# Optimization experiments

Hardware: AMD Instinct MI355X
Metric: run time of the kernel (lower is better)

The kernel has to match this reference:

```python
import jax, jax.numpy as jnp
import numpy as np

E, TOPK, D, F, FS = 16, 4, 2560, 1664, 3328
B, S = 1, 2048


def setup_inputs() -> dict:
    key = jax.random.key(0)
    ks = jax.random.split(key, 8)
    sc = lambda *sh: 1.0 / np.sqrt(sh[-2] if len(sh) > 1 else 1.0)
    return {
        "hidden_states": jax.random.normal(ks[0], (B, S, D), jnp.float32),
        "router_weight": jax.random.normal(ks[1], (E, D), jnp.float32) * (1.0 / np.sqrt(D)),
        "w_gate": jax.random.normal(ks[2], (E, D, F), jnp.float32) * (1.0 / np.sqrt(D)),
        "w_up": jax.random.normal(ks[3], (E, D, F), jnp.float32) * (1.0 / np.sqrt(D)),
        "w_down": jax.random.normal(ks[4], (E, F, D), jnp.float32) * (1.0 / np.sqrt(F)),
        "sw_gate": jax.random.normal(ks[5], (D, FS), jnp.float32) * (1.0 / np.sqrt(D)),
        "sw_up": jax.random.normal(ks[6], (D, FS), jnp.float32) * (1.0 / np.sqrt(D)),
        "sw_down": jax.random.normal(ks[7], (FS, D), jnp.float32) * (1.0 / np.sqrt(FS)),
    }


def reference(hidden_states, router_weight, w_gate, w_up, w_down, sw_gate, sw_up, sw_down):
    b, s, d = hidden_states.shape
    x = hidden_states.reshape(-1, d)  # [T, D]
    T = x.shape[0]

    # Router: linear -> softmax -> top-k -> renormalize (vLLM FusedMoE default)
    logits = x @ router_weight.T                      # [T, E]
    probs = jax.nn.softmax(logits, axis=-1)
    topk_w, topk_idx = jax.lax.top_k(probs, TOPK)     # [T, K]
    topk_w = topk_w / jnp.sum(topk_w, axis=-1, keepdims=True)
    combine = jnp.zeros((T, E), x.dtype).at[jnp.arange(T)[:, None], topk_idx].add(topk_w)  # [T, E]

    # Expert SiLU-gated MLPs (dense-dispatch reference for grouped GEMM)
    g = jnp.einsum('td,edf->tef', x, w_gate)          # [T, E, F]
    u = jnp.einsum('td,edf->tef', x, w_up)
    h = jax.nn.silu(g) * u
    y = jnp.einsum('tef,efd->ted', h, w_down)         # [T, E, D]
    sparse_out = jnp.einsum('ted,te->td', y, combine)

    # Shared expert: LlamaMLP with silu gate, no bias
    shared_out = (jax.nn.silu(x @ sw_gate) * (x @ sw_up)) @ sw_down

    return (sparse_out + shared_out).reshape(b, s, d)
```

## Files before the change

kernel.cpp:

```cpp
#include <hip/hip_runtime.h>
#include <hip/hip_bf16.h>
#include <stdint.h>

#define E_N 16
#define TOPK 4
#define DD 2560
#define FF 1664
#define FSS 3328
#define TT 2048

#define BM 128
#define BN 128
#define BK 32

typedef __attribute__((ext_vector_type(8))) __bf16 bf16x8;
typedef __attribute__((ext_vector_type(4))) float f32x4;

static_assert(DD % 64 == 0 && FF % 64 == 0 && FSS % 64 == 0, "64 divisibility");

__device__ __forceinline__ unsigned short f2bf(float f) {
  return __builtin_bit_cast(unsigned short, (__bf16)f);
}
__device__ __forceinline__ unsigned int pk2(float a, float b) {
  return (unsigned int)f2bf(a) | ((unsigned int)f2bf(b) << 16);
}

#define GLOAD16(g, l)                                                          \
  __builtin_amdgcn_global_load_lds(                                            \
      (const __attribute__((address_space(1))) void*)(g),                      \
      (__attribute__((address_space(3))) void*)(l), 16, 0, 0)

#define SBAR() __builtin_amdgcn_s_barrier()
#define SCHED0() __builtin_amdgcn_sched_barrier(0)
#define VMW(N) asm volatile("s_waitcnt vmcnt(" #N ")" ::: "memory")

__device__ __forceinline__ void swz_block(int& bm, int& bn, int& bz) {
  int gx = gridDim.x, gy = gridDim.y;
  int nwg = gx * gy * gridDim.z;
  int flat = blockIdx.x + gx * (blockIdx.y + gy * blockIdx.z);
  if ((nwg & 7) == 0) flat = (flat & 7) * (nwg >> 3) + (flat >> 3);
  bm = flat % gx;
  int rest = flat / gx;
  bn = rest % gy;
  bz = rest / gy;
}

__global__ __launch_bounds__(256) void cvt_bf16_kernel(const float* __restrict__ in,
                                                       unsigned short* __restrict__ out) {
  size_t i = ((size_t)blockIdx.x * 256 + threadIdx.x) * 4;
  float4 v = *reinterpret_cast<const float4*>(in + i);
  ushort4 o;
  o.x = f2bf(v.x); o.y = f2bf(v.y); o.z = f2bf(v.z); o.w = f2bf(v.w);
  *reinterpret_cast<ushort4*>(out + i) = o;
}

__global__ __launch_bounds__(256) void tcvt_kernel(const float* __restrict__ in,
                                                   unsigned short* __restrict__ out,
                                                   int K, int N) {
  __shared__ float lds[64 * 65];
  int z = blockIdx.z;
  in += (size_t)z * K * N;
  out += (size_t)z * K * N;
  int k0 = blockIdx.x * 64, n0 = blockIdx.y * 64;
  int t = threadIdx.x;
#pragma unroll
  for (int j = 0; j < 4; ++j) {
    int idx = j * 256 + t;
    int r = idx >> 4, c = (idx & 15) * 4;
    float4 v = *reinterpret_cast<const float4*>(in + (size_t)(k0 + r) * N + n0 + c);
    lds[r * 65 + c] = v.x;
    lds[r * 65 + c + 1] = v.y;
    lds[r * 65 + c + 2] = v.z;
    lds[r * 65 + c + 3] = v.w;
  }
  __syncthreads();
#pragma unroll
  for (int j = 0; j < 2; ++j) {
    int idx = j * 256 + t;
    int n = idx >> 3, kg = (idx & 7) * 8;
    float a0 = lds[(kg + 0) * 65 + n], a1 = lds[(kg + 1) * 65 + n];
    float a2 = lds[(kg + 2) * 65 + n], a3 = lds[(kg + 3) * 65 + n];
    float a4 = lds[(kg + 4) * 65 + n], a5 = lds[(kg + 5) * 65 + n];
    float a6 = lds[(kg + 6) * 65 + n], a7 = lds[(kg + 7) * 65 + n];
    uint4 o{pk2(a0, a1), pk2(a2, a3), pk2(a4, a5), pk2(a6, a7)};
    *reinterpret_cast<uint4*>(out + (size_t)(n0 + n) * K + k0 + kg) = o;
  }
}

__global__ __launch_bounds__(256) void router_kernel(const float* __restrict__ x,
                                                     const float* __restrict__ rw,
                                                     int* __restrict__ cnt,
                                                     int* __restrict__ list,
                                                     float* __restrict__ tw) {
  int t = blockIdx.x;
  const float* xr = x + (size_t)t * DD;
  __shared__ float logits[E_N];
  int lane = threadIdx.x & 63, wid = threadIdx.x >> 6;
  for (int ee = 0; ee < 4; ++ee) {
    int e = wid * 4 + ee;
    const float* wr = rw + (size_t)e * DD;
    float p = 0.f;
    for (int d = lane; d < DD; d += 64) p += xr[d] * wr[d];
#pragma unroll
    for (int off = 32; off > 0; off >>= 1) p += __shfl_down(p, off);
    if (lane == 0) logits[e] = p;
  }
  __syncthreads();
  if (threadIdx.x == 0) {
    float mx = -1e30f;
    for (int e = 0; e < E_N; ++e) mx = fmaxf(mx, logits[e]);
    float pe[E_N];
    for (int e = 0; e < E_N; ++e) pe[e] = __expf(logits[e] - mx);
    int idx[TOPK]; float val[TOPK]; float s4 = 0.f;
    unsigned used = 0;
    for (int k = 0; k < TOPK; ++k) {
      int bi = 0; float bv = -1.f;
      for (int e = 0; e < E_N; ++e)
        if (!((used >> e) & 1) && pe[e] > bv) { bv = pe[e]; bi = e; }
      used |= 1u << bi; idx[k] = bi; val[k] = bv; s4 += bv;
    }
    float inv = 1.f / s4;
    for (int k = 0; k < TOPK; ++k) {
      int e2 = idx[k];
      int pos = atomicAdd(&cnt[e2], 1);
      list[e2 * TT + pos] = t * 4 + k;
      tw[t * 4 + k] = val[k] * inv;
    }
  }
}

__global__ __launch_bounds__(256, 2) void gu_kernel(
    const unsigned short* __restrict__ Xb,
    const unsigned short* __restrict__ WgT,
    const unsigned short* __restrict__ WuT,
    unsigned short* __restrict__ H,
    const int* __restrict__ list, const int* __restrict__ cnt,
    int Ktot, int Ntot, int Mfixed) {
  int bm, bn, e;
  swz_block(bm, bn, e);
  int M = cnt ? cnt[e] : Mfixed;
  int m0 = bm * BM;
  if (m0 >= M) return;
  int n0 = bn * BN;
  const unsigned short* Bg0 = WgT + (size_t)e * Ktot * Ntot;
  const unsigned short* Bu0 = WuT + (size_t)e * Ktot * Ntot;
  const int* lst = list ? (list + e * TT) : nullptr;

  __shared__ __align__(16) unsigned short lds[3][12288];

  int tid = threadIdx.x, lane = tid & 63, w = tid >> 6;

  const unsigned short* pA[2];
#pragma unroll
  for (int q = 0; q < 2; ++q) {
    int J = w * 2 + q;
    int row = J * 16 + (lane >> 2);
    int c = lane & 3;
    int cs = c ^ (row & 3);
    int ar = min(m0 + row, M - 1);
    int tok = lst ? (lst[ar] >> 2) : ar;
    pA[q] = Xb + (size_t)tok * Ktot + cs * 8;
  }
  const unsigned short* pGU[4];
#pragma unroll
  for (int q = 0; q < 4; ++q) {
    int J = w * 4 + q;
    int row = J * 8 + (lane >> 3);
    int c = lane & 7;
    int sc = c ^ (row & 7);
    pGU[q] = (sc < 4) ? (Bg0 + (size_t)(n0 + row) * Ktot + sc * 8)
                      : (Bu0 + (size_t)(n0 + row) * Ktot + (sc - 4) * 8);
  }

  auto issue = [&](int kt, int buf) {
    int koff = kt * BK;
    unsigned short* dA = &lds[buf][0];
    unsigned short* dGU = &lds[buf][4096];
#pragma unroll
    for (int q = 0; q < 2; ++q)
      GLOAD16(pA[q] + koff, dA + (w * 2 + q) * 512);
#pragma unroll
    for (int q = 0; q < 4; ++q)
      GLOAD16(pGU[q] + koff, dGU + (w * 4 + q) * 512);
  };

  int wr = (w >> 1) * 64, wc = (w & 1) * 64;
  int cg = lane >> 4;
  int aoff[4], goff[4], uoff[4];
#pragma unroll
  for (int m = 0; m < 4; ++m) {
    int r = wr + m * 16 + (lane & 15);
    aoff[m] = r * 32 + ((cg ^ (r & 3)) * 8);
  }
#pragma unroll
  for (int n = 0; n < 4; ++n) {
    int r = wc + n * 16 + (lane & 15);
    goff[n] = r * 64 + ((cg ^ (r & 7)) * 8);
    uoff[n] = r * 64 + (((cg + 4) ^ (r & 7)) * 8);
  }

  f32x4 accG[4][4] = {};
  f32x4 accU[4][4] = {};

  auto compute = [&](int buf) {
    const unsigned short* A = &lds[buf][0];
    const unsigned short* GU = &lds[buf][4096];
    bf16x8 a[4], g[4], u[4];
#pragma unroll
    for (int m = 0; m < 4; ++m)
      a[m] = __builtin_bit_cast(bf16x8, *reinterpret_cast<const uint4*>(A + aoff[m]));
#pragma unroll
    for (int n = 0; n < 4; ++n) {
      g[n] = __builtin_bit_cast(bf16x8, *reinterpret_cast<const uint4*>(GU + goff[n]));
      u[n] = __builtin_bit_cast(bf16x8, *reinterpret_cast<const uint4*>(GU + uoff[n]));
    }
#pragma unroll
    for (int m = 0; m < 4; ++m)
#pragma unroll
      for (int n = 0; n < 4; ++n) {
        accG[m][n] = __builtin_amdgcn_mfma_f32_16x16x32_bf16(a[m], g[n], accG[m][n], 0, 0, 0);
        accU[m][n] = __builtin_amdgcn_mfma_f32_16x16x32_bf16(a[m], u[n], accU[m][n], 0, 0, 0);
      }
  };

  int nk = Ktot / BK;
  VMW(0); SCHED0();
  issue(0, 0);
  issue(1, 1);
  for (int kt = 0; kt < nk; ++kt) {
    if (kt + 2 < nk) { issue(kt + 2, (kt + 2) % 3); VMW(12); }
    else if (kt + 1 < nk) { VMW(6); }
    else { VMW(0); }
    SCHED0();
    SBAR(); SCHED0();
    compute(kt % 3);
    SCHED0();
    SBAR(); SCHED0();
  }

#pragma unroll
  for (int m = 0; m < 4; ++m) {
#pragma unroll
    for (int r = 0; r < 4; ++r) {
      int lr = wr + m * 16 + (lane >> 4) * 4 + r;
      int grow = m0 + lr;
      if (grow < M) {
        int code = lst ? lst[grow] : grow;
        unsigned short* Hp = H + (size_t)code * Ntot + n0 + wc + (lane & 15);
#pragma unroll
        for (int n = 0; n < 4; ++n) {
          float gg = accG[m][n][r], uu = accU[m][n][r];
          Hp[n * 16] = f2bf((gg / (1.f + __expf(-gg))) * uu);
        }
      }
    }
  }
}

__global__ __launch_bounds__(256, 3) void dn_kernel(
    const unsigned short* __restrict__ Hb,
    const unsigned short* __restrict__ WT,
    float* __restrict__ Y,
    const int* __restrict__ list, const int* __restrict__ cnt,
    const float* __restrict__ tw, int Ktot, int Ntot, int Mfixed) {
  int bm, bn, e;
  swz_block(bm, bn, e);
  int M = cnt ? cnt[e] : Mfixed;
  int m0 = bm * BM;
  if (m0 >= M) return;
  int n0 = bn * BN;
  const unsigned short* B0 = WT + (size_t)e * Ktot * Ntot;
  const int* lst = list ? (list + e * TT) : nullptr;

  __shared__ __align__(16) unsigned short lds[3][8192];

  int tid = threadIdx.x, lane = tid & 63, w = tid >> 6;

  const unsigned short* pAB[4];
#pragma unroll
  for (int q = 0; q < 4; ++q) {
    int J = w * 4 + q;
    int row = J * 8 + (lane >> 3);
    int c = lane & 7;
    int sc = c ^ (row & 7);
    if (sc < 4) {
      int ar = min(m0 + row, M - 1);
      int code = lst ? lst[ar] : ar;
      pAB[q] = Hb + (size_t)code * Ktot + sc * 8;
    } else {
      pAB[q] = B0 + (size_t)(n0 + row) * Ktot + (sc - 4) * 8;
    }
  }

  auto issue = [&](int kt, int buf) {
    int koff = kt * BK;
    unsigned short* d = &lds[buf][0];
#pragma unroll
    for (int q = 0; q < 4; ++q)
      GLOAD16(pAB[q] + koff, d + (w * 4 + q) * 512);
  };

  int wr = (w >> 1) * 64, wc = (w & 1) * 64;
  int cg = lane >> 4;
  int aoff[4], boff[4];
#pragma unroll
  for (int m = 0; m < 4; ++m) {
    int r = wr + m * 16 + (lane & 15);
    aoff[m] = r * 64 + ((cg ^ (r & 7)) * 8);
  }
#pragma unroll
  for (int n = 0; n < 4; ++n) {
    int r = wc + n * 16 + (lane & 15);
    boff[n] = r * 64 + (((cg + 4) ^ (r & 7)) * 8);
  }

  f32x4 acc[4][4] = {};

  auto compute = [&](int buf) {
    const unsigned short* AB = &lds[buf][0];
    bf16x8 a[4], b[4];
#pragma unroll
    for (int m = 0; m < 4; ++m)
      a[m] = __builtin_bit_cast(bf16x8, *reinterpret_cast<const uint4*>(AB + aoff[m]));
#pragma unroll
    for (int n = 0; n < 4; ++n)
      b[n] = __builtin_bit_cast(bf16x8, *reinterpret_cast<const uint4*>(AB + boff[n]));
#pragma unroll
    for (int m = 0; m < 4; ++m)
#pragma unroll
      for (int n = 0; n < 4; ++n)
        acc[m][n] = __builtin_amdgcn_mfma_f32_16x16x32_bf16(a[m], b[n], acc[m][n], 0, 0, 0);
  };

  int nk = Ktot / BK;
  VMW(0); SCHED0();
  issue(0, 0);
  issue(1, 1);
  for (int kt = 0; kt < nk; ++kt) {
    if (kt + 2 < nk) { issue(kt + 2, (kt + 2) % 3); VMW(8); }
    else if (kt + 1 < nk) { VMW(4); }
    else { VMW(0); }
    SCHED0();
    SBAR(); SCHED0();
    compute(kt % 3);
    SCHED0();
    SBAR(); SCHED0();
  }

#pragma unroll
  for (int m = 0; m < 4; ++m) {
#pragma unroll
    for (int r = 0; r < 4; ++r) {
      int lr = wr + m * 16 + (lane >> 4) * 4 + r;
      int grow = m0 + lr;
      if (grow < M) {
        int code = lst ? lst[grow] : grow;
        float scale = tw ? tw[code] : 1.f;
        float* Yp = Y + (size_t)code * Ntot + n0 + wc + (lane & 15);
#pragma unroll
        for (int n = 0; n < 4; ++n) Yp[n * 16] = acc[m][n][r] * scale;
      }
    }
  }
}

__global__ __launch_bounds__(256) void combine_kernel(const float* __restrict__ Y,
                                                      const float* __restrict__ Ys,
                                                      float* __restrict__ out) {
  size_t i = ((size_t)blockIdx.x * 256 + threadIdx.x) * 4;
  size_t t = i / DD;
  int d = (int)(i % DD);
  float4 a = *reinterpret_cast<const float4*>(Ys + i);
#pragma unroll
  for (int k = 0; k < 4; ++k) {
    float4 v = *reinterpret_cast<const float4*>(Y + (t * 4 + k) * (size_t)DD + d);
    a.x += v.x; a.y += v.y; a.z += v.z; a.w += v.w;
  }
  *reinterpret_cast<float4*>(out + i) = a;
}

extern "C" void kernel_launch(void* const* d_in, const int* in_sizes, int n_in,
                              void* d_out, int out_size, void* d_ws, size_t ws_size,
                              hipStream_t stream) {
  const float* x  = (const float*)d_in[0];
  const float* rw = (const float*)d_in[1];
  const float* wg = (const float*)d_in[2];
  const float* wu = (const float*)d_in[3];
  const float* wd = (const float*)d_in[4];
  const float* sg = (const float*)d_in[5];
  const float* su = (const float*)d_in[6];
  const float* sd = (const float*)d_in[7];
  float* out = (float*)d_out;

  char* ws = (char*)d_ws;
  size_t off = 0;
  auto alloc = [&](size_t bytes) {
    off = (off + 255) & ~(size_t)255;
    void* p = ws + off;
    off += bytes;
    return p;
  };
  unsigned short* W1 = (unsigned short*)alloc((size_t)E_N * FF * DD * 2);
  unsigned short* W2 = (unsigned short*)alloc((size_t)E_N * FF * DD * 2);
  unsigned short* W3 = (unsigned short*)alloc((size_t)FSS * DD * 2);
  unsigned short* W4 = (unsigned short*)alloc((size_t)FSS * DD * 2);
  unsigned short* Xb = (unsigned short*)alloc((size_t)TT * DD * 2);
  unsigned short* Hx = (unsigned short*)alloc((size_t)4 * TT * FF * 2);
  unsigned short* Hs = (unsigned short*)alloc((size_t)TT * FSS * 2);
  float* Y  = (float*)alloc((size_t)4 * TT * DD * 4);
  float* Ys = (float*)alloc((size_t)TT * DD * 4);
  float* tw = (float*)alloc((size_t)4 * TT * 4);
  int* cnt  = (int*)alloc(E_N * 4);
  int* list = (int*)alloc((size_t)E_N * TT * 4);
  (void)ws_size; (void)in_sizes; (void)n_in; (void)out_size;

  hipMemsetAsync(cnt, 0, E_N * 4, stream);
  cvt_bf16_kernel<<<TT * DD / 4 / 256, 256, 0, stream>>>(x, Xb);
  router_kernel<<<TT, 256, 0, stream>>>(x, rw, cnt, list, tw);

  tcvt_kernel<<<dim3(DD / 64, FF / 64, E_N), 256, 0, stream>>>(wg, W1, DD, FF);
  tcvt_kernel<<<dim3(DD / 64, FF / 64, E_N), 256, 0, stream>>>(wu, W2, DD, FF);
  tcvt_kernel<<<dim3(DD / 64, FSS / 64, 1), 256, 0, stream>>>(sg, W3, DD, FSS);
  tcvt_kernel<<<dim3(DD / 64, FSS / 64, 1), 256, 0, stream>>>(su, W4, DD, FSS);

  gu_kernel<<<dim3(TT / BM, FF / BN, E_N), 256, 0, stream>>>(
      Xb, W1, W2, Hx, list, cnt, DD, FF, 0);
  gu_kernel<<<dim3(TT / BM, FSS / BN, 1), 256, 0, stream>>>(
      Xb, W3, W4, Hs, nullptr, nullptr, DD, FSS, TT);

  tcvt_kernel<<<dim3(FF / 64, DD / 64, E_N), 256, 0, stream>>>(wd, W1, FF, DD);
  tcvt_kernel<<<dim3(FSS / 64, DD / 64, 1), 256, 0, stream>>>(sd, W2, FSS, DD);

  dn_kernel<<<dim3(TT / BM, DD / BN, E_N), 256, 0, stream>>>(
      Hx, W1, Y, list, cnt, tw, FF, DD, 0);
  dn_kernel<<<dim3(TT / BM, DD / BN, 1), 256, 0, stream>>>(
      Hs, W2, Ys, nullptr, nullptr, nullptr, FSS, DD, TT);

  combine_kernel<<<TT * DD / 4 / 256, 256, 0, stream>>>(Y, Ys, out);
}
```

Baseline: 1.036 ms.

## Enlarge GEMM tiles to 512-thread blocks with 4-stage pipeline and MFMA priority

Moves the gate/up and down grouped GEMMs to 512-thread blocks (8 waves) with larger tiles: 256x128 for gate/up and 128x256 for down. The shared-memory layout becomes a simpler per-thread row-major swizzle. The load pipeline deepens from 3 to 4 LDS stages, and s_setprio raises wave priority around the MFMA sections. The goal is more data reuse per loaded byte and better latency hiding. In exchange, LDS use rises, fewer blocks fit per CU, and padding waste grows for experts with small token counts. The grid's M dimension is also widened to TT*4 per expert, which launches many blocks that exit immediately.

```diff
diff --git a/kernel.cpp b/kernel.cpp
--- a/kernel.cpp
+++ b/kernel.cpp
@@ -9,14 +9,10 @@
 #define FSS 3328
 #define TT 2048
 
-#define BM 128
-#define BN 128
 #define BK 32
 
 typedef __attribute__((ext_vector_type(8))) __bf16 bf16x8;
 typedef __attribute__((ext_vector_type(4))) float f32x4;
-
-static_assert(DD % 64 == 0 && FF % 64 == 0 && FSS % 64 == 0, "64 divisibility");
 
 __device__ __forceinline__ unsigned short f2bf(float f) {
   return __builtin_bit_cast(unsigned short, (__bf16)f);
@@ -129,7 +125,7 @@
   }
 }
 
-__global__ __launch_bounds__(256, 2) void gu_kernel(
+__global__ __launch_bounds__(512, 2) void gu_kernel(
     const unsigned short* __restrict__ Xb,
     const unsigned short* __restrict__ WgT,
     const unsigned short* __restrict__ WuT,
@@ -139,125 +135,114 @@
   int bm, bn, e;
   swz_block(bm, bn, e);
   int M = cnt ? cnt[e] : Mfixed;
-  int m0 = bm * BM;
+  int m0 = bm * 256;
   if (m0 >= M) return;
-  int n0 = bn * BN;
+  int n0 = bn * 128;
   const unsigned short* Bg0 = WgT + (size_t)e * Ktot * Ntot;
   const unsigned short* Bu0 = WuT + (size_t)e * Ktot * Ntot;
   const int* lst = list ? (list + e * TT) : nullptr;
 
-  __shared__ __align__(16) unsigned short lds[3][12288];
+  __shared__ __align__(16) unsigned short lds[4][16384];
 
   int tid = threadIdx.x, lane = tid & 63, w = tid >> 6;
-
-  const unsigned short* pA[2];
-#pragma unroll
-  for (int q = 0; q < 2; ++q) {
-    int J = w * 2 + q;
-    int row = J * 16 + (lane >> 2);
-    int c = lane & 3;
-    int cs = c ^ (row & 3);
-    int ar = min(m0 + row, M - 1);
-    int tok = lst ? (lst[ar] >> 2) : ar;
-    pA[q] = Xb + (size_t)tok * Ktot + cs * 8;
-  }
-  const unsigned short* pGU[4];
-#pragma unroll
-  for (int q = 0; q < 4; ++q) {
-    int J = w * 4 + q;
-    int row = J * 8 + (lane >> 3);
-    int c = lane & 7;
-    int sc = c ^ (row & 7);
-    pGU[q] = (sc < 4) ? (Bg0 + (size_t)(n0 + row) * Ktot + sc * 8)
-                      : (Bu0 + (size_t)(n0 + row) * Ktot + (sc - 4) * 8);
+  int wm = w >> 1, wn = w & 1;
+
+  const unsigned short* sp[4];
+  {
+    int rh = tid >> 2, c = tid & 3;
+    int cs = (c ^ ((rh >> 1) & 3)) * 8;
+    int a0 = min(m0 + rh, M - 1), a1 = min(m0 + 128 + rh, M - 1);
+    int t0 = lst ? (lst[a0] >> 2) : a0;
+    int t1 = lst ? (lst[a1] >> 2) : a1;
+    sp[0] = Xb + (size_t)t0 * Ktot + cs;
+    sp[1] = Xb + (size_t)t1 * Ktot + cs;
+    sp[2] = Bg0 + (size_t)(n0 + rh) * Ktot + cs;
+    sp[3] = Bu0 + (size_t)(n0 + rh) * Ktot + cs;
   }
 
   auto issue = [&](int kt, int buf) {
     int koff = kt * BK;
-    unsigned short* dA = &lds[buf][0];
-    unsigned short* dGU = &lds[buf][4096];
-#pragma unroll
-    for (int q = 0; q < 2; ++q)
-      GLOAD16(pA[q] + koff, dA + (w * 2 + q) * 512);
-#pragma unroll
-    for (int q = 0; q < 4; ++q)
-      GLOAD16(pGU[q] + koff, dGU + (w * 4 + q) * 512);
+    unsigned short* d = &lds[buf][0];
+#pragma unroll
+    for (int j = 0; j < 4; ++j)
+      GLOAD16(sp[j] + koff, d + j * 4096 + tid * 8);
   };
 
-  int wr = (w >> 1) * 64, wc = (w & 1) * 64;
   int cg = lane >> 4;
-  int aoff[4], goff[4], uoff[4];
-#pragma unroll
-  for (int m = 0; m < 4; ++m) {
-    int r = wr + m * 16 + (lane & 15);
-    aoff[m] = r * 32 + ((cg ^ (r & 3)) * 8);
-  }
-#pragma unroll
-  for (int n = 0; n < 4; ++n) {
-    int r = wc + n * 16 + (lane & 15);
-    goff[n] = r * 64 + ((cg ^ (r & 7)) * 8);
-    uoff[n] = r * 64 + (((cg + 4) ^ (r & 7)) * 8);
+  int aoff[4], goff[4];
+#pragma unroll
+  for (int mf = 0; mf < 4; ++mf) {
+    int r = wm * 64 + mf * 16 + (lane & 15);
+    aoff[mf] = r * 32 + ((cg ^ ((r >> 1) & 3)) * 8);
+  }
+#pragma unroll
+  for (int nf = 0; nf < 4; ++nf) {
+    int rb = wn * 64 + nf * 16 + (lane & 15);
+    goff[nf] = 8192 + rb * 32 + ((cg ^ ((rb >> 1) & 3)) * 8);
   }
 
   f32x4 accG[4][4] = {};
   f32x4 accU[4][4] = {};
 
   auto compute = [&](int buf) {
-    const unsigned short* A = &lds[buf][0];
-    const unsigned short* GU = &lds[buf][4096];
+    const unsigned short* L = &lds[buf][0];
     bf16x8 a[4], g[4], u[4];
 #pragma unroll
-    for (int m = 0; m < 4; ++m)
-      a[m] = __builtin_bit_cast(bf16x8, *reinterpret_cast<const uint4*>(A + aoff[m]));
-#pragma unroll
-    for (int n = 0; n < 4; ++n) {
-      g[n] = __builtin_bit_cast(bf16x8, *reinterpret_cast<const uint4*>(GU + goff[n]));
-      u[n] = __builtin_bit_cast(bf16x8, *reinterpret_cast<const uint4*>(GU + uoff[n]));
+    for (int mf = 0; mf < 4; ++mf)
+      a[mf] = __builtin_bit_cast(bf16x8, *reinterpret_cast<const uint4*>(L + aoff[mf]));
+#pragma unroll
+    for (int nf = 0; nf < 4; ++nf) {
+      g[nf] = __builtin_bit_cast(bf16x8, *reinterpret_cast<const uint4*>(L + goff[nf]));
+      u[nf] = __builtin_bit_cast(bf16x8, *reinterpret_cast<const uint4*>(L + goff[nf] + 4096));
     }
-#pragma unroll
-    for (int m = 0; m < 4; ++m)
-#pragma unroll
-      for (int n = 0; n < 4; ++n) {
-        accG[m][n] = __builtin_amdgcn_mfma_f32_16x16x32_bf16(a[m], g[n], accG[m][n], 0, 0, 0);
-        accU[m][n] = __builtin_amdgcn_mfma_f32_16x16x32_bf16(a[m], u[n], accU[m][n], 0, 0, 0);
+    __builtin_amdgcn_s_setprio(1);
+#pragma unroll
+    for (int mf = 0; mf < 4; ++mf)
+#pragma unroll
+      for (int nf = 0; nf < 4; ++nf) {
+        accG[mf][nf] = __builtin_amdgcn_mfma_f32_16x16x32_bf16(a[mf], g[nf], accG[mf][nf], 0, 0, 0);
+        accU[mf][nf] = __builtin_amdgcn_mfma_f32_16x16x32_bf16(a[mf], u[nf], accU[mf][nf], 0, 0, 0);
       }
+    __builtin_amdgcn_s_setprio(0);
   };
 
   int nk = Ktot / BK;
-  VMW(0); SCHED0();
   issue(0, 0);
   issue(1, 1);
+  issue(2, 2);
   for (int kt = 0; kt < nk; ++kt) {
-    if (kt + 2 < nk) { issue(kt + 2, (kt + 2) % 3); VMW(12); }
-    else if (kt + 1 < nk) { VMW(6); }
+    int rem = nk - 1 - kt;
+    if (rem >= 3) { issue(kt + 3, (kt + 3) & 3); VMW(12); }
+    else if (rem == 2) { VMW(8); }
+    else if (rem == 1) { VMW(4); }
     else { VMW(0); }
     SCHED0();
     SBAR(); SCHED0();
-    compute(kt % 3);
+    compute(kt & 3);
     SCHED0();
     SBAR(); SCHED0();
   }
 
 #pragma unroll
-  for (int m = 0; m < 4; ++m) {
-#pragma unroll
-    for (int r = 0; r < 4; ++r) {
-      int lr = wr + m * 16 + (lane >> 4) * 4 + r;
+  for (int mf = 0; mf < 4; ++mf) {
+#pragma unroll
+    for (int q = 0; q < 4; ++q) {
+      int lr = wm * 64 + mf * 16 + (lane >> 4) * 4 + q;
       int grow = m0 + lr;
       if (grow < M) {
         int code = lst ? lst[grow] : grow;
-        unsigned short* Hp = H + (size_t)code * Ntot + n0 + wc + (lane & 15);
-#pragma unroll
-        for (int n = 0; n < 4; ++n) {
-          float gg = accG[m][n][r], uu = accU[m][n][r];
-          Hp[n * 16] = f2bf((gg / (1.f + __expf(-gg))) * uu);
+        unsigned short* Hp = H + (size_t)code * Ntot + n0 + wn * 64 + (lane & 15);
+#pragma unroll
+        for (int nf = 0; nf < 4; ++nf) {
+          float gg = accG[mf][nf][q], uu = accU[mf][nf][q];
+          Hp[nf * 16] = f2bf((gg / (1.f + __expf(-gg))) * uu);
         }
       }
     }
   }
 }
 
-__global__ __launch_bounds__(256, 3) void dn_kernel(
+__global__ __launch_bounds__(512, 2) void dn_kernel(
     const unsigned short* __restrict__ Hb,
     const unsigned short* __restrict__ WT,
     float* __restrict__ Y,
@@ -266,99 +251,98 @@
   int bm, bn, e;
   swz_block(bm, bn, e);
   int M = cnt ? cnt[e] : Mfixed;
-  int m0 = bm * BM;
+  int m0 = bm * 128;
   if (m0 >= M) return;
-  int n0 = bn * BN;
+  int n0 = bn * 256;
   const unsigned short* B0 = WT + (size_t)e * Ktot * Ntot;
   const int* lst = list ? (list + e * TT) : nullptr;
 
-  __shared__ __align__(16) unsigned short lds[3][8192];
+  __shared__ __align__(16) unsigned short lds[4][12288];
 
   int tid = threadIdx.x, lane = tid & 63, w = tid >> 6;
-
-  const unsigned short* pAB[4];
-#pragma unroll
-  for (int q = 0; q < 4; ++q) {
-    int J = w * 4 + q;
-    int row = J * 8 + (lane >> 3);
-    int c = lane & 7;
-    int sc = c ^ (row & 7);
-    if (sc < 4) {
-      int ar = min(m0 + row, M - 1);
-      int code = lst ? lst[ar] : ar;
-      pAB[q] = Hb + (size_t)code * Ktot + sc * 8;
-    } else {
-      pAB[q] = B0 + (size_t)(n0 + row) * Ktot + (sc - 4) * 8;
-    }
+  int wm = w >> 2, wn = w & 3;
+
+  const unsigned short* sp[3];
+  {
+    int rh = tid >> 2, c = tid & 3;
+    int cs = (c ^ ((rh >> 1) & 3)) * 8;
+    int a0 = min(m0 + rh, M - 1);
+    int code0 = lst ? lst[a0] : a0;
+    sp[0] = Hb + (size_t)code0 * Ktot + cs;
+    sp[1] = B0 + (size_t)(n0 + rh) * Ktot + cs;
+    sp[2] = B0 + (size_t)(n0 + 128 + rh) * Ktot + cs;
   }
 
   auto issue = [&](int kt, int buf) {
     int koff = kt * BK;
     unsigned short* d = &lds[buf][0];
 #pragma unroll
-    for (int q = 0; q < 4; ++q)
-      GLOAD16(pAB[q] + koff, d + (w * 4 + q) * 512);
+    for (int j = 0; j < 3; ++j)
+      GLOAD16(sp[j] + koff, d + j * 4096 + tid * 8);
   };
 
-  int wr = (w >> 1) * 64, wc = (w & 1) * 64;
   int cg = lane >> 4;
   int aoff[4], boff[4];
 #pragma unroll
-  for (int m = 0; m < 4; ++m) {
-    int r = wr + m * 16 + (lane & 15);
-    aoff[m] = r * 64 + ((cg ^ (r & 7)) * 8);
-  }
-#pragma unroll
-  for (int n = 0; n < 4; ++n) {
-    int r = wc + n * 16 + (lane & 15);
-    boff[n] = r * 64 + (((cg + 4) ^ (r & 7)) * 8);
+  for (int mf = 0; mf < 4; ++mf) {
+    int r = wm * 64 + mf * 16 + (lane & 15);
+    aoff[mf] = r * 32 + ((cg ^ ((r >> 1) & 3)) * 8);
+  }
+#pragma unroll
+  for (int nf = 0; nf < 4; ++nf) {
+    int rb = wn * 64 + nf * 16 + (lane & 15);
+    boff[nf] = 4096 + rb * 32 + ((cg ^ ((rb >> 1) & 3)) * 8);
   }
 
   f32x4 acc[4][4] = {};
 
   auto compute = [&](int buf) {
-    const unsigned short* AB = &lds[buf][0];
+    const unsigned short* L = &lds[buf][0];
     bf16x8 a[4], b[4];
 #pragma unroll
-    for (int m = 0; m < 4; ++m)
-      a[m] = __builtin_bit_cast(bf16x8, *reinterpret_cast<const uint4*>(AB + aoff[m]));
-#pragma unroll
-    for (int n = 0; n < 4; ++n)
-      b[n] = __builtin_bit_cast(bf16x8, *reinterpret_cast<const uint4*>(AB + boff[n]));
-#pragma unroll
-    for (int m = 0; m < 4; ++m)
-#pragma unroll
-      for (int n = 0; n < 4; ++n)
-        acc[m][n] = __builtin_amdgcn_mfma_f32_16x16x32_bf16(a[m], b[n], acc[m][n], 0, 0, 0);
+    for (int mf = 0; mf < 4; ++mf)
+      a[mf] = __builtin_bit_cast(bf16x8, *reinterpret_cast<const uint4*>(L + aoff[mf]));
+#pragma unroll
+    for (int nf = 0; nf < 4; ++nf)
+      b[nf] = __builtin_bit_cast(bf16x8, *reinterpret_cast<const uint4*>(L + boff[nf]));
+    __builtin_amdgcn_s_setprio(1);
+#pragma unroll
+    for (int mf = 0; mf < 4; ++mf)
+#pragma unroll
+      for (int nf = 0; nf < 4; ++nf)
+        acc[mf][nf] = __builtin_amdgcn_mfma_f32_16x16x32_bf16(a[mf], b[nf], acc[mf][nf], 0, 0, 0);
+    __builtin_amdgcn_s_setprio(0);
   };
 
   int nk = Ktot / BK;
-  VMW(0); SCHED0();
   issue(0, 0);
   issue(1, 1);
+  issue(2, 2);
   for (int kt = 0; kt < nk; ++kt) {
-    if (kt + 2 < nk) { issue(kt + 2, (kt + 2) % 3); VMW(8); }
-    else if (kt + 1 < nk) { VMW(4); }
+    int rem = nk - 1 - kt;
+    if (rem >= 3) { issue(kt + 3, (kt + 3) & 3); VMW(9); }
+    else if (rem == 2) { VMW(6); }
+    else if (rem == 1) { VMW(3); }
     else { VMW(0); }
     SCHED0();
     SBAR(); SCHED0();
-    compute(kt % 3);
+    compute(kt & 3);
     SCHED0();
     SBAR(); SCHED0();
   }
 
 #pragma unroll
-  for (int m = 0; m < 4; ++m) {
-#pragma unroll
-    for (int r = 0; r < 4; ++r) {
-      int lr = wr + m * 16 + (lane >> 4) * 4 + r;
+  for (int mf = 0; mf < 4; ++mf) {
+#pragma unroll
+    for (int q = 0; q < 4; ++q) {
+      int lr = wm * 64 + mf * 16 + (lane >> 4) * 4 + q;
       int grow = m0 + lr;
       if (grow < M) {
         int code = lst ? lst[grow] : grow;
         float scale = tw ? tw[code] : 1.f;
-        float* Yp = Y + (size_t)code * Ntot + n0 + wc + (lane & 15);
-#pragma unroll
-        for (int n = 0; n < 4; ++n) Yp[n * 16] = acc[m][n][r] * scale;
+        float* Yp = Y + (size_t)code * Ntot + n0 + wn * 64 + (lane & 15);
+#pragma unroll
+        for (int nf = 0; nf < 4; ++nf) Yp[nf * 16] = acc[mf][nf][q] * scale;
       }
     }
   }
@@ -423,17 +407,17 @@
   tcvt_kernel<<<dim3(DD / 64, FSS / 64, 1), 256, 0, stream>>>(sg, W3, DD, FSS);
   tcvt_kernel<<<dim3(DD / 64, FSS / 64, 1), 256, 0, stream>>>(su, W4, DD, FSS);
 
-  gu_kernel<<<dim3(TT / BM, FF / BN, E_N), 256, 0, stream>>>(
+  gu_kernel<<<dim3(TT * 4 / 256, FF / 128, E_N), 512, 0, stream>>>(
       Xb, W1, W2, Hx, list, cnt, DD, FF, 0);
-  gu_kernel<<<dim3(TT / BM, FSS / BN, 1), 256, 0, stream>>>(
+  gu_kernel<<<dim3(TT / 256, FSS / 128, 1), 512, 0, stream>>>(
       Xb, W3, W4, Hs, nullptr, nullptr, DD, FSS, TT);
 
   tcvt_kernel<<<dim3(FF / 64, DD / 64, E_N), 256, 0, stream>>>(wd, W1, FF, DD);
   tcvt_kernel<<<dim3(FSS / 64, DD / 64, 1), 256, 0, stream>>>(sd, W2, FSS, DD);
 
-  dn_kernel<<<dim3(TT / BM, DD / BN, E_N), 256, 0, stream>>>(
+  dn_kernel<<<dim3(TT * 4 / 128, DD / 256, E_N), 512, 0, stream>>>(
       Hx, W1, Y, list, cnt, tw, FF, DD, 0);
-  dn_kernel<<<dim3(TT / BM, DD / BN, 1), 256, 0, stream>>>(
+  dn_kernel<<<dim3(TT / 128, DD / 256, 1), 512, 0, stream>>>(
       Hs, W2, Ys, nullptr, nullptr, nullptr, FSS, DD, TT);
 
   combine_kernel<<<TT * DD / 4 / 256, 256, 0, stream>>>(Y, Ys, out);
```

Measured after the change: 1.159 ms. 11.9% more time.
